# Kernel tuning notes

Measured on AMD Instinct MI355X. Metric: run time of the kernel, lower is better.

The kernel has to match this reference:

```python
import jax, jax.numpy as jnp
from jax import lax
import numpy as np

SCALE = 4.0  # InputEmbedding scale


def lstm_cell(x, h, c, W_ih, W_hh, b_ih, b_hh):
    # torch.nn.LSTMCell math: gate order i, f, g, o
    gates = x @ W_ih.T + b_ih + h @ W_hh.T + b_hh
    i, f, g, o = jnp.split(gates, 4, axis=-1)
    c_new = jax.nn.sigmoid(f) * c + jax.nn.sigmoid(i) * jnp.tanh(g)
    h_new = jax.nn.sigmoid(o) * jnp.tanh(c_new)
    return h_new, c_new


def setup_inputs() -> dict:
    key = jax.random.key(0)
    ks = jax.random.split(key, 6)
    B, T, N, H, E = 1024, 256, 1, 256, 128
    s = 0.05
    return dict(
        observed=jax.random.normal(ks[0], (B, T, N, 2), jnp.float32),
        pooled=jax.random.normal(ks[1], (B, T, 32), jnp.float32),
        W_emb=jax.random.normal(ks[2], (2, E - 2), jnp.float32) * s,
        b_emb=jnp.zeros((E - 2,), jnp.float32),
        W_ih=jax.random.normal(ks[3], (4 * H, E), jnp.float32) * s,
        W_hh=jax.random.normal(ks[4], (4 * H, H), jnp.float32) * s,
        b_ih=jnp.zeros((4 * H,), jnp.float32),
        b_hh=jnp.zeros((4 * H,), jnp.float32),
    )


def reference(observed, pooled, W_emb, b_emb, W_ih, W_hh, b_ih, b_hh):
    # observed: (B, T, N=1, 2); pooled unused since pool=None
    B, T, N, _ = observed.shape
    H = W_hh.shape[1]
    E = W_ih.shape[1]
    obs = observed[:, :, 0, :]                       # (B, T, 2) track 0
    vel = obs[:, 1:] - obs[:, :-1]                   # (B, T-1, 2) obs2 - obs1
    # InputEmbedding: relu(Linear(vel*scale)) with 2-wide zero tag slot
    emb = jax.nn.relu((vel * SCALE) @ W_emb + b_emb)  # (B, T-1, E-2)
    inp = jnp.concatenate([emb, jnp.zeros((B, T - 1, 2), emb.dtype)], axis=-1)
    # start_enc tag: zeros(E-2) ++ [1, 0]
    tag = jnp.zeros((B, E), emb.dtype).at[:, E - 2].set(1.0)
    h0 = jnp.zeros((B, H), emb.dtype)
    c0 = jnp.zeros((B, H), emb.dtype)
    h, c = lstm_cell(tag, h0, c0, W_ih, W_hh, b_ih, b_hh)  # tag_step

    def step(carry, x_t):
        h, c = carry
        h, c = lstm_cell(x_t, h, c, W_ih, W_hh, b_ih, b_hh)
        return (h, c), None

    (h, c), _ = lax.scan(step, (h, c), jnp.swapaxes(inp, 0, 1))  # scan over T-1
    return h, c
```

## Files before the change

kernel.cpp:

```cpp
#include <hip/hip_runtime.h>
#include <stdint.h>


typedef float  f32x4  __attribute__((ext_vector_type(4)));
typedef float  f32x2  __attribute__((ext_vector_type(2)));
typedef short  bf16x8 __attribute__((ext_vector_type(8)));
typedef short  bf16x4 __attribute__((ext_vector_type(4)));
typedef unsigned int u32x4 __attribute__((ext_vector_type(4)));

#define T_STEPS 255
#define ROWB    80
#define FRAGB   1296
#define XT(b)   ((b)*4*FRAGB)
#define HT(b)   (10368 + (b)*8*FRAGB)
#define RB_OFF  31104
#define WM_OFF  47488
#define H1_OFF  49408
#define C1_OFF  50432
#define SMEM_SZ 52224

#define AG_ST(p, v) __hip_atomic_store((p), (v), __ATOMIC_RELAXED, __HIP_MEMORY_SCOPE_AGENT)
#define AG_LD(p)    __hip_atomic_load((p),        __ATOMIC_RELAXED, __HIP_MEMORY_SCOPE_AGENT)

__device__ __forceinline__ unsigned short f2bf(float f){
  union { float f; unsigned int u; } v; v.f = f;
  unsigned int u = v.u;
  return (unsigned short)((u + 0x7fffu + ((u >> 16) & 1u)) >> 16);
}
__device__ __forceinline__ float sigf(float x){
  float e = __builtin_amdgcn_exp2f(-1.4426950408889634f * x);
  return __builtin_amdgcn_rcpf(1.0f + e);
}
__device__ __forceinline__ float tanh_(float x){
  float e = __builtin_amdgcn_exp2f(-2.8853900817779268f * x);
  return (1.0f - e) * __builtin_amdgcn_rcpf(1.0f + e);
}

__global__ void zero_ws(unsigned int* flags, unsigned int* outw){
  const unsigned idx = blockIdx.x*512u + threadIdx.x;
  if (idx < 16384u)        AG_ST(flags + idx, 0u);
  else if (idx < 540672u)  AG_ST(outw + (idx - 16384u), 0u);
}

__global__ void __launch_bounds__(512, 2)
lstm_k(const float* __restrict__ obs,
       const float* __restrict__ Wemb, const float* __restrict__ Bemb,
       const float* __restrict__ Wih,  const float* __restrict__ Whh,
       const float* __restrict__ bih,  const float* __restrict__ bhh,
       float* out, unsigned int* flags, unsigned int* hbuf)
{
  __shared__ __align__(16) char smem[SMEM_SZ];
  const int tid  = threadIdx.x;
  const int l    = tid & 63;
  const int w    = tid >> 6;
  const int hsub = w & 3;
  const int kh   = w >> 2;
  const int lc   = l & 15;
  const int lg   = l >> 4;
  const int T    = blockIdx.x & 63;
  const int q    = blockIdx.x >> 6;

  unsigned xcc;
  asm volatile("s_getreg_b32 %0, hwreg(HW_REG_XCC_ID)" : "=s"(xcc));
  bool fast;
  {
    volatile unsigned* xs = (volatile unsigned*)(smem + WM_OFF);
    if (tid == 0) AG_ST(flags + (T*4 + q)*16 + 8, 1u + xcc);
    if (tid < 4){
      unsigned v; long g = 0;
      do { v = AG_LD(flags + (T*4 + tid)*16 + 8); } while (v == 0 && ++g < 10000000L);
      xs[tid] = v;
    }
    __syncthreads();
    unsigned ok = 1;
    #pragma unroll
    for (int j = 0; j < 4; ++j) ok &= (xs[j] == 1u + xcc) ? 1u : 0u;
    __syncthreads();
    if (tid == 0) AG_ST(flags + (T*4 + q)*16 + 9, ok ? 2u : 1u);
    if (tid < 4){
      unsigned v; long g = 0;
      do { v = AG_LD(flags + (T*4 + tid)*16 + 9); } while (v == 0 && ++g < 10000000L);
      xs[tid] = v;
    }
    __syncthreads();
    unsigned all2 = 1;
    #pragma unroll
    for (int j = 0; j < 4; ++j) all2 &= (xs[j] == 2u) ? 1u : 0u;
    fast = (all2 != 0);
    __syncthreads();
  }

  bf16x8 wf[4][6];
  #pragma unroll
  for (int g = 0; g < 4; ++g){
    const int rowg = g*256 + q*64 + hsub*16 + lc;
    #pragma unroll
    for (int kfl = 0; kfl < 6; ++kfl){
      const float* src;
      if (kfl < 2){
        const int k0 = (kh*2 + kfl)*32 + lg*8;
        src = Wih + rowg*128 + k0;
      } else {
        const int k0 = (kh*4 + kfl - 2)*32 + lg*8;
        src = Whh + rowg*256 + k0;
      }
      f32x4 s0 = *(const f32x4*)(src);
      f32x4 s1 = *(const f32x4*)(src + 4);
      bf16x8 v;
      v[0]=(short)f2bf(s0[0]); v[1]=(short)f2bf(s0[1]);
      v[2]=(short)f2bf(s0[2]); v[3]=(short)f2bf(s0[3]);
      v[4]=(short)f2bf(s1[0]); v[5]=(short)f2bf(s1[1]);
      v[6]=(short)f2bf(s1[2]); v[7]=(short)f2bf(s1[3]);
      wf[g][kfl] = v;
    }
  }
  float bias[4];
  #pragma unroll
  for (int g = 0; g < 4; ++g){
    const int rowg = g*256 + q*64 + hsub*16 + lc;
    bias[g] = (kh == 0) ? (bih[rowg] + bhh[rowg]) : 0.f;
  }

  float* wm0 = (float*)(smem + WM_OFF);
  float* wm1 = wm0 + 160;
  float* bem = wm0 + 320;
  if (tid < 128){
    float a = 0.f, b = 0.f, c = 0.f;
    if (tid < 126){ a = 4.0f*Wemb[tid]; b = 4.0f*Wemb[126 + tid]; c = Bemb[tid]; }
    const int pi = tid + (tid >> 4)*4;
    wm0[pi] = a; wm1[pi] = b; bem[pi] = c;
  }
  float* h1f = (float*)(smem + H1_OFF);
  float* c1f = (float*)(smem + C1_OFF);
  if (tid < 256){
    const int j = tid;
    float gi  = Wih[(j      )*128 + 126] + bih[j      ] + bhh[j      ];
    float gg2 = Wih[(512 + j)*128 + 126] + bih[512 + j] + bhh[512 + j];
    float go  = Wih[(768 + j)*128 + 126] + bih[768 + j] + bhh[768 + j];
    float c1 = sigf(gi)*tanh_(gg2);
    h1f[j] = sigf(go)*tanh_(c1); c1f[j] = c1;
  }
  __syncthreads();

  auto xtile = [&](int buf, float vx, float vy){
    const int row = tid >> 5;
    const int cb  = (tid & 31) * 4;
    const int cp  = cb + (cb >> 4)*4;
    f32x4 wa = *(const f32x4*)(wm0 + cp);
    f32x4 wc = *(const f32x4*)(wm1 + cp);
    f32x4 ba = *(const f32x4*)(bem + cp);
    bf16x4 v;
    #pragma unroll
    for (int i = 0; i < 4; ++i)
      v[i] = (short)f2bf(fmaxf(vx*wa[i] + vy*wc[i] + ba[i], 0.f));
    *(bf16x4*)(smem + XT(buf) + (cb >> 5)*FRAGB + row*ROWB + (cb & 31)*2) = v;
  };

  const int gr = tid >> 5;
  const int c8 = (tid & 31) * 8;

  const int col  = q*64 + hsub*16 + lc;
  const int row0 = lg*4 + 2*kh;
  float cs0, cs1;
  { float cv = c1f[col]; cs0 = cv; cs1 = cv; }
  {
    bf16x8 v;
    #pragma unroll
    for (int i = 0; i < 8; ++i) v[i] = (short)f2bf(h1f[c8 + i]);
    *(bf16x8*)(smem + HT(0) + (c8 >> 5)*FRAGB + gr*ROWB + (c8 & 31)*2) = v;
  }
  {
    const float* op = obs + (T*16 + (tid >> 5))*512;
    f32x2 p0 = *(const f32x2*)(op), p1 = *(const f32x2*)(op + 2);
    xtile(0, p1[0] - p0[0], p1[1] - p0[1]);
  }
  __syncthreads();

  float hv0 = 0.f, hv1 = 0.f;
  long guard = 0;

  for (int t = 0; t < T_STEPS; ++t){
    const int cur = t & 1;
    const int rowA = lc;
    f32x4 acc0 = (f32x4){bias[0],bias[0],bias[0],bias[0]};
    f32x4 acc1 = (f32x4){bias[1],bias[1],bias[1],bias[1]};
    f32x4 acc2 = (f32x4){bias[2],bias[2],bias[2],bias[2]};
    f32x4 acc3 = (f32x4){bias[3],bias[3],bias[3],bias[3]};
    #pragma unroll
    for (int kfl = 0; kfl < 2; ++kfl){
      const char* pa = smem + XT(cur) + (kh*2 + kfl)*FRAGB + rowA*ROWB + lg*16;
      bf16x8 a = *(const bf16x8*)pa;
      acc0 = __builtin_amdgcn_mfma_f32_16x16x32_bf16(a, wf[0][kfl], acc0, 0, 0, 0);
      acc1 = __builtin_amdgcn_mfma_f32_16x16x32_bf16(a, wf[1][kfl], acc1, 0, 0, 0);
      acc2 = __builtin_amdgcn_mfma_f32_16x16x32_bf16(a, wf[2][kfl], acc2, 0, 0, 0);
      acc3 = __builtin_amdgcn_mfma_f32_16x16x32_bf16(a, wf[3][kfl], acc3, 0, 0, 0);
    }

    if (t > 0){
      const unsigned want = ((unsigned)t) << 16;
      const unsigned int* src = hbuf + cur*262144 + T*4096 + gr*256 + c8;
      u32x4 q0, q1;
      unsigned bad;
      do {
        if (fast){
          asm volatile("global_load_dwordx4 %0, %2, off sc0 nt\n\t"
                       "global_load_dwordx4 %1, %2, off offset:16 sc0 nt\n\t"
                       "s_waitcnt vmcnt(0)"
                       : "=&v"(q0), "=&v"(q1) : "v"(src) : "memory");
        } else {
          #pragma unroll
          for (int i = 0; i < 4; ++i){
            q0[i] = AG_LD(src + i); q1[i] = AG_LD(src + 4 + i);
          }
        }
        bad = 0;
        #pragma unroll
        for (int i = 0; i < 4; ++i){
          bad |= (q0[i] ^ want) & 0xffff0000u;
          bad |= (q1[i] ^ want) & 0xffff0000u;
        }
      } while (bad && ++guard < 2000000L);

      bf16x8 v;
      #pragma unroll
      for (int i = 0; i < 4; ++i){
        v[i]     = (short)(q0[i] & 0xffffu);
        v[4 + i] = (short)(q1[i] & 0xffffu);
      }
      *(bf16x8*)(smem + HT(cur) + (c8 >> 5)*FRAGB + gr*ROWB + (c8 & 31)*2) = v;
    }

    if (t < T_STEPS - 1){
      const float* op = obs + (T*16 + (tid >> 5))*512 + (t + 1)*2;
      f32x2 p0 = *(const f32x2*)(op), p1 = *(const f32x2*)(op + 2);
      xtile(cur ^ 1, p1[0] - p0[0], p1[1] - p0[1]);
    }
    __syncthreads();

    #pragma unroll
    for (int kfl = 2; kfl < 6; ++kfl){
      const char* pa = smem + HT(cur) + (kh*4 + kfl - 2)*FRAGB + rowA*ROWB + lg*16;
      bf16x8 a = *(const bf16x8*)pa;
      acc0 = __builtin_amdgcn_mfma_f32_16x16x32_bf16(a, wf[0][kfl], acc0, 0, 0, 0);
      acc1 = __builtin_amdgcn_mfma_f32_16x16x32_bf16(a, wf[1][kfl], acc1, 0, 0, 0);
      acc2 = __builtin_amdgcn_mfma_f32_16x16x32_bf16(a, wf[2][kfl], acc2, 0, 0, 0);
      ac3:;
      acc3 = __builtin_amdgcn_mfma_f32_16x16x32_bf16(a, wf[3][kfl], acc3, 0, 0, 0);
    }
    {
      f32x2* rb = (f32x2*)(smem + RB_OFF);
      const int sl = kh ^ 1;
      const int base = ((hsub*2 + sl)*4)*64 + l;
      f32x2 e0, e1, e2, e3;
      if (kh == 0){
        e0 = (f32x2){acc0[2], acc0[3]}; e1 = (f32x2){acc1[2], acc1[3]};
        e2 = (f32x2){acc2[2], acc2[3]}; e3 = (f32x2){acc3[2], acc3[3]};
      } else {
        e0 = (f32x2){acc0[0], acc0[1]}; e1 = (f32x2){acc1[0], acc1[1]};
        e2 = (f32x2){acc2[0], acc2[1]}; e3 = (f32x2){acc3[0], acc3[1]};
      }
      rb[base] = e0; rb[base + 64] = e1; rb[base + 128] = e2; rb[base + 192] = e3;
    }
    __syncthreads();
    {
      f32x2* rb = (f32x2*)(smem + RB_OFF);
      const int base = ((hsub*2 + kh)*4)*64 + l;
      f32x2 r0 = rb[base], r1 = rb[base + 64], r2 = rb[base + 128], r3 = rb[base + 192];
      float gi0, gi1, gf0, gf1, gg0, gg1, go0, go1;
      if (kh == 0){
        gi0 = acc0[0] + r0[0]; gi1 = acc0[1] + r0[1];
        gf0 = acc1[0] + r1[0]; gf1 = acc1[1] + r1[1];
        gg0 = acc2[0] + r2[0]; gg1 = acc2[1] + r2[1];
        go0 = acc3[0] + r3[0]; go1 = acc3[1] + r3[1];
      } else {
        gi0 = acc0[2] + r0[0]; gi1 = acc0[3] + r0[1];
        gf0 = acc1[2] + r1[0]; gf1 = acc1[3] + r1[1];
        gg0 = acc2[2] + r2[0]; gg1 = acc2[3] + r2[1];
        go0 = acc3[2] + r3[0]; go1 = acc3[3] + r3[1];
      }
      cs0 = sigf(gf0)*cs0 + sigf(gi0)*tanh_(gg0);
      hv0 = sigf(go0)*tanh_(cs0);
      cs1 = sigf(gf1)*cs1 + sigf(gi1)*tanh_(gg1);
      hv1 = sigf(go1)*tanh_(cs1);
    }

    if (t < T_STEPS - 1){
      const unsigned want2 = ((unsigned)(t + 1)) << 16;
      unsigned w0 = want2 | f2bf(hv0);
      unsigned w1 = want2 | f2bf(hv1);
      unsigned int* dst = hbuf + (cur ^ 1)*262144 + T*4096 + row0*256 + col;
      if (fast){
        asm volatile("global_store_dword %0, %1, off sc0\n\t"
                     "global_store_dword %0, %2, off offset:1024 sc0"
                     :: "v"(dst), "v"(w0), "v"(w1) : "memory");
      } else {
        AG_ST(dst, w0); AG_ST(dst + 256, w1);
      }
    }
  }

  if (tid == 0) AG_ST(flags + (T*4 + q)*16 + 10, 1u);
  if (tid < 4){
    unsigned v; long g = 0;
    do { v = AG_LD(flags + (T*4 + tid)*16 + 10); } while (v == 0 && ++g < 10000000L);
  }
  __syncthreads();

  {
    const int r = T*16 + row0;
    out[r*256 + col]                = hv0;
    out[(r + 1)*256 + col]          = hv1;
    out[262144 + r*256 + col]       = cs0;
    out[262144 + (r + 1)*256 + col] = cs1;
  }
}

extern "C" void kernel_launch(void* const* d_in, const int* in_sizes, int n_in,
                              void* d_out, int out_size, void* d_ws, size_t ws_size,
                              hipStream_t stream) {
  (void)in_sizes; (void)n_in; (void)out_size; (void)ws_size;
  const float* obs  = (const float*)d_in[0];
  const float* Wemb = (const float*)d_in[2];
  const float* Bemb = (const float*)d_in[3];
  const float* Wih  = (const float*)d_in[4];
  const float* Whh  = (const float*)d_in[5];
  const float* bih  = (const float*)d_in[6];
  const float* bhh  = (const float*)d_in[7];
  float* out = (float*)d_out;
  unsigned int* flags = (unsigned int*)d_ws;
  unsigned int* hbuf  = (unsigned int*)d_out;

  zero_ws<<<dim3(1056), dim3(512), 0, stream>>>(flags, hbuf);
  lstm_k<<<dim3(256), dim3(512), 0, stream>>>(obs, Wemb, Bemb, Wih, Whh, bih, bhh,
                                              out, flags, hbuf);
}
```

Measured before the change: 464.0 us.

## Unroll recurrence by two, issue h gather before MFMAs, prefetch observations

The time loop is unrolled by two through a macro, so buffer offsets and global pointers become compile-time constants. The first polling load of the previous hidden state is issued before the input-projection MFMAs and the embedding tile, hiding its latency, with a retry loop only on a tag mismatch. Observation values are loaded one step ahead, and bf16 conversion uses packed v_cvt_pk_bf16_f32 instructions, which may round differently from the manual rounding. The fragment stride is changed from 1296 to 1312 bytes, shifting the LDS layout and possibly its bank-conflict pattern.

```diff
diff --git a/kernel.cpp b/kernel.cpp
--- a/kernel.cpp
+++ b/kernel.cpp
@@ -5,18 +5,18 @@
 typedef float  f32x4  __attribute__((ext_vector_type(4)));
 typedef float  f32x2  __attribute__((ext_vector_type(2)));
 typedef short  bf16x8 __attribute__((ext_vector_type(8)));
-typedef short  bf16x4 __attribute__((ext_vector_type(4)));
 typedef unsigned int u32x4 __attribute__((ext_vector_type(4)));
+typedef unsigned int u32x2 __attribute__((ext_vector_type(2)));
 
 #define T_STEPS 255
 #define ROWB    80
-#define FRAGB   1296
-#define XT(b)   ((b)*4*FRAGB)
-#define HT(b)   (10368 + (b)*8*FRAGB)
-#define RB_OFF  31104
-#define WM_OFF  47488
-#define H1_OFF  49408
-#define C1_OFF  50432
+#define FRAGB   1312
+#define XTO(b)  ((b)*4*FRAGB)
+#define HTO(b)  (10496 + (b)*8*FRAGB)
+#define RB_OFF  31488
+#define WM_OFF  47872
+#define H1_OFF  49792
+#define C1_OFF  50816
 #define SMEM_SZ 52224
 
 #define AG_ST(p, v) __hip_atomic_store((p), (v), __ATOMIC_RELAXED, __HIP_MEMORY_SCOPE_AGENT)
@@ -142,162 +142,185 @@
   }
   __syncthreads();
 
-  auto xtile = [&](int buf, float vx, float vy){
-    const int row = tid >> 5;
-    const int cb  = (tid & 31) * 4;
-    const int cp  = cb + (cb >> 4)*4;
-    f32x4 wa = *(const f32x4*)(wm0 + cp);
-    f32x4 wc = *(const f32x4*)(wm1 + cp);
-    f32x4 ba = *(const f32x4*)(bem + cp);
-    bf16x4 v;
-    #pragma unroll
-    for (int i = 0; i < 4; ++i)
-      v[i] = (short)f2bf(fmaxf(vx*wa[i] + vy*wc[i] + ba[i], 0.f));
-    *(bf16x4*)(smem + XT(buf) + (cb >> 5)*FRAGB + row*ROWB + (cb & 31)*2) = v;
-  };
-
   const int gr = tid >> 5;
   const int c8 = (tid & 31) * 8;
-
   const int col  = q*64 + hsub*16 + lc;
   const int row0 = lg*4 + 2*kh;
+  const float* obs_base = obs + (T*16 + gr)*512;
+  char* const xwb   = smem + (((tid & 31)*4) >> 5)*FRAGB + gr*ROWB + (((tid & 31)*4) & 31)*2;
+  const int  xcp    = ((tid & 31)*4) + (((tid & 31)*4) >> 4)*4;
+  char* const gwb   = smem + (c8 >> 5)*FRAGB + gr*ROWB + (c8 & 31)*2;
+  const char* const abx = smem + kh*2*FRAGB + lc*ROWB + lg*16;
+  const char* const abh = smem + kh*4*FRAGB + lc*ROWB + lg*16;
+  f32x2* const rb = (f32x2*)(smem + RB_OFF);
+  const int rb_exp = (hsub*2 + (kh ^ 1))*256 + l;
+  const int rb_red = (hsub*2 + kh)*256 + l;
+  unsigned int* const dstP[2] = { hbuf + 262144 + T*4096 + row0*256 + col,
+                                  hbuf +          T*4096 + row0*256 + col };
+  const unsigned int* const srcP[2] = { hbuf +          T*4096 + gr*256 + c8,
+                                        hbuf + 262144 + T*4096 + gr*256 + c8 };
+
+  auto xtile = [&](int buf, float vx, float vy){
+    f32x4 wa = *(const f32x4*)(wm0 + xcp);
+    f32x4 wc = *(const f32x4*)(wm1 + xcp);
+    f32x4 ba = *(const f32x4*)(bem + xcp);
+    float e0 = fmaxf(vx*wa[0] + vy*wc[0] + ba[0], 0.f);
+    float e1 = fmaxf(vx*wa[1] + vy*wc[1] + ba[1], 0.f);
+    float e2 = fmaxf(vx*wa[2] + vy*wc[2] + ba[2], 0.f);
+    float e3 = fmaxf(vx*wa[3] + vy*wc[3] + ba[3], 0.f);
+    unsigned lo, hi;
+    asm("v_cvt_pk_bf16_f32 %0, %1, %2" : "=v"(lo) : "v"(e0), "v"(e1));
+    asm("v_cvt_pk_bf16_f32 %0, %1, %2" : "=v"(hi) : "v"(e2), "v"(e3));
+    *(u32x2*)(xwb + XTO(0) + buf*XTO(1)) = (u32x2){lo, hi};
+  };
+
   float cs0, cs1;
   { float cv = c1f[col]; cs0 = cv; cs1 = cv; }
   {
     bf16x8 v;
     #pragma unroll
     for (int i = 0; i < 8; ++i) v[i] = (short)f2bf(h1f[c8 + i]);
-    *(bf16x8*)(smem + HT(0) + (c8 >> 5)*FRAGB + gr*ROWB + (c8 & 31)*2) = v;
+    *(bf16x8*)(gwb + HTO(0)) = v;
   }
   {
-    const float* op = obs + (T*16 + (tid >> 5))*512;
-    f32x2 p0 = *(const f32x2*)(op), p1 = *(const f32x2*)(op + 2);
+    f32x2 p0 = *(const f32x2*)(obs_base), p1 = *(const f32x2*)(obs_base + 2);
     xtile(0, p1[0] - p0[0], p1[1] - p0[1]);
   }
+  f32x2 pc0 = *(const f32x2*)(obs_base + 2);
+  f32x2 pc1 = *(const f32x2*)(obs_base + 4);
   __syncthreads();
 
   float hv0 = 0.f, hv1 = 0.f;
   long guard = 0;
 
-  for (int t = 0; t < T_STEPS; ++t){
-    const int cur = t & 1;
-    const int rowA = lc;
-    f32x4 acc0 = (f32x4){bias[0],bias[0],bias[0],bias[0]};
-    f32x4 acc1 = (f32x4){bias[1],bias[1],bias[1],bias[1]};
-    f32x4 acc2 = (f32x4){bias[2],bias[2],bias[2],bias[2]};
-    f32x4 acc3 = (f32x4){bias[3],bias[3],bias[3],bias[3]};
-    #pragma unroll
-    for (int kfl = 0; kfl < 2; ++kfl){
-      const char* pa = smem + XT(cur) + (kh*2 + kfl)*FRAGB + rowA*ROWB + lg*16;
-      bf16x8 a = *(const bf16x8*)pa;
-      acc0 = __builtin_amdgcn_mfma_f32_16x16x32_bf16(a, wf[0][kfl], acc0, 0, 0, 0);
-      acc1 = __builtin_amdgcn_mfma_f32_16x16x32_bf16(a, wf[1][kfl], acc1, 0, 0, 0);
-      acc2 = __builtin_amdgcn_mfma_f32_16x16x32_bf16(a, wf[2][kfl], acc2, 0, 0, 0);
-      acc3 = __builtin_amdgcn_mfma_f32_16x16x32_bf16(a, wf[3][kfl], acc3, 0, 0, 0);
-    }
-
-    if (t > 0){
-      const unsigned want = ((unsigned)t) << 16;
-      const unsigned int* src = hbuf + cur*262144 + T*4096 + gr*256 + c8;
-      u32x4 q0, q1;
-      unsigned bad;
-      do {
-        if (fast){
-          asm volatile("global_load_dwordx4 %0, %2, off sc0 nt\n\t"
-                       "global_load_dwordx4 %1, %2, off offset:16 sc0 nt\n\t"
-                       "s_waitcnt vmcnt(0)"
-                       : "=&v"(q0), "=&v"(q1) : "v"(src) : "memory");
-        } else {
-          #pragma unroll
-          for (int i = 0; i < 4; ++i){
-            q0[i] = AG_LD(src + i); q1[i] = AG_LD(src + 4 + i);
-          }
-        }
-        bad = 0;
-        #pragma unroll
-        for (int i = 0; i < 4; ++i){
-          bad |= (q0[i] ^ want) & 0xffff0000u;
-          bad |= (q1[i] ^ want) & 0xffff0000u;
-        }
-      } while (bad && ++guard < 2000000L);
-
-      bf16x8 v;
-      #pragma unroll
-      for (int i = 0; i < 4; ++i){
-        v[i]     = (short)(q0[i] & 0xffffu);
-        v[4 + i] = (short)(q1[i] & 0xffffu);
-      }
-      *(bf16x8*)(smem + HT(cur) + (c8 >> 5)*FRAGB + gr*ROWB + (c8 & 31)*2) = v;
-    }
-
-    if (t < T_STEPS - 1){
-      const float* op = obs + (T*16 + (tid >> 5))*512 + (t + 1)*2;
-      f32x2 p0 = *(const f32x2*)(op), p1 = *(const f32x2*)(op + 2);
-      xtile(cur ^ 1, p1[0] - p0[0], p1[1] - p0[1]);
-    }
-    __syncthreads();
-
-    #pragma unroll
-    for (int kfl = 2; kfl < 6; ++kfl){
-      const char* pa = smem + HT(cur) + (kh*4 + kfl - 2)*FRAGB + rowA*ROWB + lg*16;
-      bf16x8 a = *(const bf16x8*)pa;
-      acc0 = __builtin_amdgcn_mfma_f32_16x16x32_bf16(a, wf[0][kfl], acc0, 0, 0, 0);
-      acc1 = __builtin_amdgcn_mfma_f32_16x16x32_bf16(a, wf[1][kfl], acc1, 0, 0, 0);
-      acc2 = __builtin_amdgcn_mfma_f32_16x16x32_bf16(a, wf[2][kfl], acc2, 0, 0, 0);
-      ac3:;
-      acc3 = __builtin_amdgcn_mfma_f32_16x16x32_bf16(a, wf[3][kfl], acc3, 0, 0, 0);
-    }
-    {
-      f32x2* rb = (f32x2*)(smem + RB_OFF);
-      const int sl = kh ^ 1;
-      const int base = ((hsub*2 + sl)*4)*64 + l;
-      f32x2 e0, e1, e2, e3;
-      if (kh == 0){
-        e0 = (f32x2){acc0[2], acc0[3]}; e1 = (f32x2){acc1[2], acc1[3]};
-        e2 = (f32x2){acc2[2], acc2[3]}; e3 = (f32x2){acc3[2], acc3[3]};
-      } else {
-        e0 = (f32x2){acc0[0], acc0[1]}; e1 = (f32x2){acc1[0], acc1[1]};
-        e2 = (f32x2){acc2[0], acc2[1]}; e3 = (f32x2){acc3[0], acc3[1]};
-      }
-      rb[base] = e0; rb[base + 64] = e1; rb[base + 128] = e2; rb[base + 192] = e3;
-    }
-    __syncthreads();
-    {
-      f32x2* rb = (f32x2*)(smem + RB_OFF);
-      const int base = ((hsub*2 + kh)*4)*64 + l;
-      f32x2 r0 = rb[base], r1 = rb[base + 64], r2 = rb[base + 128], r3 = rb[base + 192];
-      float gi0, gi1, gf0, gf1, gg0, gg1, go0, go1;
-      if (kh == 0){
-        gi0 = acc0[0] + r0[0]; gi1 = acc0[1] + r0[1];
-        gf0 = acc1[0] + r1[0]; gf1 = acc1[1] + r1[1];
-        gg0 = acc2[0] + r2[0]; gg1 = acc2[1] + r2[1];
-        go0 = acc3[0] + r3[0]; go1 = acc3[1] + r3[1];
-      } else {
-        gi0 = acc0[2] + r0[0]; gi1 = acc0[3] + r0[1];
-        gf0 = acc1[2] + r1[0]; gf1 = acc1[3] + r1[1];
-        gg0 = acc2[2] + r2[0]; gg1 = acc2[3] + r2[1];
-        go0 = acc3[2] + r3[0]; go1 = acc3[3] + r3[1];
-      }
-      cs0 = sigf(gf0)*cs0 + sigf(gi0)*tanh_(gg0);
-      hv0 = sigf(go0)*tanh_(cs0);
-      cs1 = sigf(gf1)*cs1 + sigf(gi1)*tanh_(gg1);
-      hv1 = sigf(go1)*tanh_(cs1);
-    }
-
-    if (t < T_STEPS - 1){
-      const unsigned want2 = ((unsigned)(t + 1)) << 16;
-      unsigned w0 = want2 | f2bf(hv0);
-      unsigned w1 = want2 | f2bf(hv1);
-      unsigned int* dst = hbuf + (cur ^ 1)*262144 + T*4096 + row0*256 + col;
-      if (fast){
-        asm volatile("global_store_dword %0, %1, off sc0\n\t"
-                     "global_store_dword %0, %2, off offset:1024 sc0"
-                     :: "v"(dst), "v"(w0), "v"(w1) : "memory");
-      } else {
-        AG_ST(dst, w0); AG_ST(dst + 256, w1);
-      }
-    }
-  }
+#define STEP(CUR, tv, DO_GATHER)                                                     \
+  {                                                                                  \
+    u32x4 q0, q1;                                                                    \
+    if (DO_GATHER && fast){                                                          \
+      asm volatile("global_load_dwordx4 %0, %2, off sc0 nt\n\t"                      \
+                   "global_load_dwordx4 %1, %2, off offset:16 sc0 nt"                \
+                   : "=&v"(q0), "=&v"(q1) : "v"(srcP[CUR]) : "memory");              \
+    }                                                                                \
+    f32x4 acc0 = (f32x4){bias[0],bias[0],bias[0],bias[0]};                           \
+    f32x4 acc1 = (f32x4){bias[1],bias[1],bias[1],bias[1]};                           \
+    f32x4 acc2 = (f32x4){bias[2],bias[2],bias[2],bias[2]};                           \
+    f32x4 acc3 = (f32x4){bias[3],bias[3],bias[3],bias[3]};                           \
+    _Pragma("unroll")                                                                \
+    for (int kfl = 0; kfl < 2; ++kfl){                                               \
+      bf16x8 a = *(const bf16x8*)(abx + XTO(CUR) + kfl*FRAGB);                       \
+      acc0 = __builtin_amdgcn_mfma_f32_16x16x32_bf16(a, wf[0][kfl], acc0, 0, 0, 0);  \
+      acc1 = __builtin_amdgcn_mfma_f32_16x16x32_bf16(a, wf[1][kfl], acc1, 0, 0, 0);  \
+      acc2 = __builtin_amdgcn_mfma_f32_16x16x32_bf16(a, wf[2][kfl], acc2, 0, 0, 0);  \
+      acc3 = __builtin_amdgcn_mfma_f32_16x16x32_bf16(a, wf[3][kfl], acc3, 0, 0, 0);  \
+    }                                                                                \
+    if ((tv) < T_STEPS - 1){                                                         \
+      float vx = pc1[0] - pc0[0], vy = pc1[1] - pc0[1];                              \
+      xtile((CUR) ^ 1, vx, vy);                                                      \
+    }                                                                                \
+    if (DO_GATHER){                                                                  \
+      const unsigned want = ((unsigned)(tv)) << 16;                                  \
+      unsigned bad;                                                                  \
+      if (fast){                                                                     \
+        asm volatile("s_waitcnt vmcnt(0)" : "+v"(q0), "+v"(q1) :: "memory");         \
+        unsigned x = (q0[0]^want)|(q0[1]^want)|(q0[2]^want)|(q0[3]^want)             \
+                   | (q1[0]^want)|(q1[1]^want)|(q1[2]^want)|(q1[3]^want);            \
+        bad = x & 0xffff0000u;                                                       \
+        while (bad && ++guard < 2000000L){                                           \
+          asm volatile("global_load_dwordx4 %0, %2, off sc0 nt\n\t"                  \
+                       "global_load_dwordx4 %1, %2, off offset:16 sc0 nt\n\t"        \
+                       "s_waitcnt vmcnt(0)"                                          \
+                       : "=&v"(q0), "=&v"(q1) : "v"(srcP[CUR]) : "memory");          \
+          x = (q0[0]^want)|(q0[1]^want)|(q0[2]^want)|(q0[3]^want)                    \
+            | (q1[0]^want)|(q1[1]^want)|(q1[2]^want)|(q1[3]^want);                   \
+          bad = x & 0xffff0000u;                                                     \
+        }                                                                            \
+      } else {                                                                       \
+        do {                                                                         \
+          _Pragma("unroll")                                                          \
+          for (int i = 0; i < 4; ++i){                                               \
+            q0[i] = AG_LD(srcP[CUR] + i); q1[i] = AG_LD(srcP[CUR] + 4 + i);          \
+          }                                                                          \
+          unsigned x = (q0[0]^want)|(q0[1]^want)|(q0[2]^want)|(q0[3]^want)           \
+                     | (q1[0]^want)|(q1[1]^want)|(q1[2]^want)|(q1[3]^want);          \
+          bad = x & 0xffff0000u;                                                     \
+        } while (bad && ++guard < 2000000L);                                         \
+      }                                                                              \
+      unsigned d0 = (q0[0] & 0xffffu) | (q0[1] << 16);                               \
+      unsigned d1 = (q0[2] & 0xffffu) | (q0[3] << 16);                               \
+      unsigned d2 = (q1[0] & 0xffffu) | (q1[1] << 16);                               \
+      unsigned d3 = (q1[2] & 0xffffu) | (q1[3] << 16);                               \
+      *(u32x4*)(gwb + HTO(CUR)) = (u32x4){d0, d1, d2, d3};                           \
+    }                                                                                \
+    if ((tv) < T_STEPS - 2){                                                         \
+      pc0 = *(const f32x2*)(obs_base + ((tv) + 2)*2);                                \
+      pc1 = *(const f32x2*)(obs_base + ((tv) + 2)*2 + 2);                            \
+    }                                                                                \
+    __syncthreads();                         \
+    _Pragma("unroll")                                                                \
+    for (int kfl = 2; kfl < 6; ++kfl){                                               \
+      bf16x8 a = *(const bf16x8*)(abh + HTO(CUR) + (kfl - 2)*FRAGB);                 \
+      acc0 = __builtin_amdgcn_mfma_f32_16x16x32_bf16(a, wf[0][kfl], acc0, 0, 0, 0);  \
+      acc1 = __builtin_amdgcn_mfma_f32_16x16x32_bf16(a, wf[1][kfl], acc1, 0, 0, 0);  \
+      acc2 = __builtin_amdgcn_mfma_f32_16x16x32_bf16(a, wf[2][kfl], acc2, 0, 0, 0);  \
+      acc3 = __builtin_amdgcn_mfma_f32_16x16x32_bf16(a, wf[3][kfl], acc3, 0, 0, 0);  \
+    }                                                                                \
+    {                                                                                \
+      f32x2 e0, e1, e2, e3;                                                          \
+      if (kh == 0){                                                                  \
+        e0 = (f32x2){acc0[2], acc0[3]}; e1 = (f32x2){acc1[2], acc1[3]};              \
+        e2 = (f32x2){acc2[2], acc2[3]}; e3 = (f32x2){acc3[2], acc3[3]};              \
+      } else {                                                                       \
+        e0 = (f32x2){acc0[0], acc0[1]}; e1 = (f32x2){acc1[0], acc1[1]};              \
+        e2 = (f32x2){acc2[0], acc2[1]}; e3 = (f32x2){acc3[0], acc3[1]};              \
+      }                                                                              \
+      rb[rb_exp] = e0; rb[rb_exp + 64] = e1;                                         \
+      rb[rb_exp + 128] = e2; rb[rb_exp + 192] = e3;                                  \
+    }                                                                                \
+    __syncthreads();                                                  \
+    {                                                                                \
+      f32x2 r0 = rb[rb_red], r1 = rb[rb_red + 64];                                   \
+      f32x2 r2 = rb[rb_red + 128], r3 = rb[rb_red + 192];                            \
+      float gi0, gi1, gf0, gf1, gg0, gg1, go0, go1;                                  \
+      if (kh == 0){                                                                  \
+        gi0 = acc0[0] + r0[0]; gi1 = acc0[1] + r0[1];                                \
+        gf0 = acc1[0] + r1[0]; gf1 = acc1[1] + r1[1];                                \
+        gg0 = acc2[0] + r2[0]; gg1 = acc2[1] + r2[1];                                \
+        go0 = acc3[0] + r3[0]; go1 = acc3[1] + r3[1];                                \
+      } else {                                                                       \
+        gi0 = acc0[2] + r0[0]; gi1 = acc0[3] + r0[1];                                \
+        gf0 = acc1[2] + r1[0]; gf1 = acc1[3] + r1[1];                                \
+        gg0 = acc2[2] + r2[0]; gg1 = acc2[3] + r2[1];                                \
+        go0 = acc3[2] + r3[0]; go1 = acc3[3] + r3[1];                                \
+      }                                                                              \
+      cs0 = sigf(gf0)*cs0 + sigf(gi0)*tanh_(gg0);                                    \
+      hv0 = sigf(go0)*tanh_(cs0);                                                    \
+      cs1 = sigf(gf1)*cs1 + sigf(gi1)*tanh_(gg1);                                    \
+      hv1 = sigf(go1)*tanh_(cs1);                                                    \
+    }                                                                                \
+    if ((tv) < T_STEPS - 1){                                                         \
+      const unsigned want2 = ((unsigned)((tv) + 1)) << 16;                           \
+      unsigned pk;                                                                   \
+      asm("v_cvt_pk_bf16_f32 %0, %1, %2" : "=v"(pk) : "v"(hv0), "v"(hv1));           \
+      unsigned w0 = want2 | (pk & 0xffffu);                                          \
+      unsigned w1 = want2 | (pk >> 16);                                              \
+      if (fast){                                                                     \
+        asm volatile("global_store_dword %0, %1, off sc0\n\t"                        \
+                     "global_store_dword %0, %2, off offset:1024 sc0"                \
+                     :: "v"(dstP[CUR]), "v"(w0), "v"(w1) : "memory");                \
+      } else {                                                                       \
+        AG_ST(dstP[CUR], w0); AG_ST(dstP[CUR] + 256, w1);                            \
+      }                                                                              \
+    }                                                                                \
+  }
+
+  STEP(0, 0, 0)
+  for (int t = 1; t < 253; t += 2){
+    STEP(1, t, 1)
+    STEP(0, t + 1, 1)
+  }
+  STEP(1, 253, 1)
+  STEP(0, 254, 1)
+#undef STEP
 
   if (tid == 0) AG_ST(flags + (T*4 + q)*16 + 10, 1u);
   if (tid < 4){
```

Result: faster. 386.7 us (median of 2 runs) (-16.7%).
